# Kernel optimization log

Hardware: AMD Instinct MI355X
Metric: run time of the kernel (lower is better)

## Reference

```python
import jax, jax.numpy as jnp
import numpy as np


def _causal_kernel_mask(K):
    # casual_mask[i, K-i:] = 0 for i in 1..p
    p = K // 2
    m = np.ones((p + 1, K), np.float32)
    for i in range(1, p + 1):
        m[i, K - i:] = 0.0
    return jnp.asarray(m)


def setup_inputs() -> dict:
    rng = jax.random.key(0)
    k0, k1, k2, k3, k4 = jax.random.split(rng, 5)
    B, H, N, F = 2, 16, 1024, 64
    V, K = 32000, 5
    return {
        "input_ids": jax.random.randint(k0, (B, N), 0, V),
        "query": jax.random.normal(k1, (B, H, N, F), dtype=jnp.float32),
        "key": jax.random.normal(k2, (B, H, N, F), dtype=jnp.float32),
        "value": jax.random.normal(k3, (B, H, N, F), dtype=jnp.float32),
        "emb_weight": jax.random.normal(k4, (V, 2 * K), dtype=jnp.float32) * 0.02,
    }


def reference(input_ids, query, key, value, emb_weight):
    B, H, N, F = query.shape
    K = emb_weight.shape[1] // 2  # head/layer invariant -> emb dim = 2*K
    p = K // 2
    G = 2 * H

    # ---- get_kernel (layer 0; head_invariant + layer_invariant) ----
    kern = emb_weight[input_ids]                       # [B,N,2K]
    kern = kern.reshape(B, N, 2, 1, K)                 # [B,N,2,1,K]
    kern = jnp.broadcast_to(kern, (B, N, 2, H, K)).reshape(B, N, G, K)

    # ---- conv_key_value (for_casual=True, strict_on_casual=True) ----
    kv = jnp.concatenate([key, value], axis=1)         # [B,2H,N,F]
    kv_pad = jnp.pad(kv, ((0, 0), (0, 0), (p, p), (0, 0)))
    # unfold over token dim: [B,2H,K,N,F]
    kv_unf = jnp.stack([kv_pad[:, :, k:k + N, :] for k in range(K)], axis=2)
    cmask = _causal_kernel_mask(K)                     # [p+1,K]
    kern_m = kern[:, :, :, None, :] * cmask[None, None, None]  # [B,N,2H,p+1,K]
    # dynamic depthwise conv with per-offset causal masking
    out = jnp.einsum('bgknf,bngjk->bgjnf', kv_unf, kern_m)     # [B,2H,p+1,N,F]
    key_c = out[:, :H, 0]                              # [B,H,N,F]
    value_c = out[:, H:, 0]                            # [B,H,N,F]

    # ---- attention with causal-boundary corrections (n_past = 0) ----
    scale = 1.0 / jnp.sqrt(jnp.asarray(F, dtype=query.dtype))
    q = query * scale
    scores = jnp.einsum('bhnf,bhmf->bhnm', q, key_c)   # [B,H,N,N]

    # correct_attn_weights_near_casual_boundary
    for i in range(p):
        off = p - 1 - i
        cb_key = out[:, :H, 1 + i]                     # [B,H,N,F]
        corr = jnp.einsum('bhnf,bhnf->bhn', q[:, :, off:, :], cb_key[:, :, :N - off, :])
        rows = jnp.arange(N - off) + off
        cols = jnp.arange(N - off)
        scores = scores.at[:, :, rows, cols].set(corr)

    causal = jnp.tril(jnp.ones((N, N), dtype=bool))
    scores = jnp.where(causal, scores, jnp.asarray(-1e9, dtype=scores.dtype))
    probs = jax.nn.softmax(scores, axis=-1)
    attn = jnp.einsum('bhnm,bhmf->bhnf', probs, value_c)

    # correct_attn_output_near_casual_boundary
    for i in range(p):
        off = p - 1 - i
        cb_value = out[:, H:, 1 + i]                   # [B,H,N,F]
        idx = jnp.arange(N - off)
        diag_w = probs[:, :, idx + off, idx]           # diag offset=-off: [B,H,N-off]
        diff_v = cb_value[:, :, :N - off, :] - value_c[:, :, :N - off, :]
        diff = diag_w[..., None] * diff_v
        attn = attn + jnp.pad(diff, ((0, 0), (0, 0), (off, 0), (0, 0)))

    return attn
```

## Files before the change

kernel.cpp:

```cpp
#include <hip/hip_runtime.h>

#define HD    64
#define NSEQ  1024
#define NPB   12
#define CROWS 32
#define LOG2E 1.44269504088896f

typedef __attribute__((ext_vector_type(8))) __bf16 bf16x8;
typedef __attribute__((ext_vector_type(4))) float  f32x4;
typedef __attribute__((ext_vector_type(4))) unsigned short u16x4;

__device__ __constant__ unsigned char PAIRS12[NPB] = {
    6, 8, 10, 12, 14, 15, 4, 13, 2, 11, 0, 9 };

__device__ inline unsigned short f2bf(float x) {
    unsigned u = __float_as_uint(x);
    return (unsigned short)((u + 0x7fffu + ((u >> 16) & 1u)) >> 16);
}
__device__ inline unsigned pk2(float a, float b) {
    return (unsigned)f2bf(a) | ((unsigned)f2bf(b) << 16);
}
__device__ inline float dot4(f32x4 a, f32x4 b) {
    return a.x * b.x + a.y * b.y + a.z * b.z + a.w * b.w;
}

__global__ __launch_bounds__(256) void conv_kernel(
    const int* __restrict__ ids,
    const float* __restrict__ keyg,
    const float* __restrict__ valg,
    const float* __restrict__ qg,
    const float* __restrict__ emb,
    unsigned short* __restrict__ kc,
    unsigned short* __restrict__ vcT,
    float* __restrict__ dg1, float* __restrict__ dg2)
{
    __shared__ float se[(CROWS + 1) * 10];
    __shared__ float vtile[CROWS][68];
    int pid = blockIdx.x;
    int bh = pid & 31;
    int n0 = (pid >> 5) * CROWS;
    int b  = bh >> 4;
    int t  = threadIdx.x;
    size_t hb = (size_t)bh * NSEQ * HD;

    for (int u = t; u < (CROWS + 1) * 10; u += 256) {
        int r = u / 10, c = u - r * 10;
        int n = n0 - 1 + r;
        se[u] = (n >= 0) ? emb[(size_t)ids[b * NSEQ + n] * 10 + c] : 0.f;
    }
    __syncthreads();

    const float* kb = keyg + hb;
    const float* vb = valg + hb;
#pragma unroll
    for (int i = 0; i < 2; ++i) {
        int u  = (i << 8) + t;
        int nl = u >> 4, g4 = u & 15;
        int n  = n0 + nl, f = g4 << 2;
        const float* e  = se + (nl + 1) * 10;
        const float* ep = se + nl * 10;
        f32x4 xk[5], xv[5];
#pragma unroll
        for (int k = 0; k < 5; ++k) {
            int m = n + k - 2;
            if (m >= 0 && m < NSEQ) {
                xk[k] = *(const f32x4*)(kb + (size_t)m * HD + f);
                xv[k] = *(const f32x4*)(vb + (size_t)m * HD + f);
            } else {
                xk[k] = (f32x4){0.f, 0.f, 0.f, 0.f};
                xv[k] = (f32x4){0.f, 0.f, 0.f, 0.f};
            }
        }
        f32x4 km3 = (n >= 3) ? *(const f32x4*)(kb + (size_t)(n - 3) * HD + f)
                             : (f32x4){0.f, 0.f, 0.f, 0.f};
        f32x4 qv = *(const f32x4*)(qg + hb + (size_t)n * HD + f) * (0.125f * LOG2E);

        f32x4 k012 = e[0] * xk[0] + e[1] * xk[1] + e[2] * xk[2];
        f32x4 kcv  = k012 + e[3] * xk[3] + e[4] * xk[4];
        f32x4 vcv  = e[5] * xv[0] + e[6] * xv[1] + e[7] * xv[2] + e[8] * xv[3] + e[9] * xv[4];

        u16x4 kq;
        kq.x = f2bf(kcv.x); kq.y = f2bf(kcv.y); kq.z = f2bf(kcv.z); kq.w = f2bf(kcv.w);
        *(u16x4*)(kc + hb + (size_t)n * HD + f) = kq;
        *(f32x4*)(&vtile[nl][f]) = vcv;

        float s2 = dot4(qv, k012);
        f32x4 kj1 = ep[0] * km3 + ep[1] * xk[0] + ep[2] * xk[1] + ep[3] * xk[2];
        float s1 = dot4(qv, kj1);
#pragma unroll
        for (int o = 1; o < 16; o <<= 1) {
            s2 += __shfl_xor(s2, o, 64);
            s1 += __shfl_xor(s1, o, 64);
        }
        if (g4 == 0) {
            dg2[bh * NSEQ + n] = s2;
            dg1[bh * NSEQ + n] = s1;
        }
    }
    __syncthreads();
#pragma unroll
    for (int i = 0; i < 2; ++i) {
        int u = (i << 8) + t;
        int f = u >> 3, nn = (u & 7) << 2;
        u16x4 o;
        o.x = f2bf(vtile[nn + 0][f]);
        o.y = f2bf(vtile[nn + 1][f]);
        o.z = f2bf(vtile[nn + 2][f]);
        o.w = f2bf(vtile[nn + 3][f]);
        *(u16x4*)(vcT + ((size_t)bh * HD + f) * NSEQ + n0 + nn) = o;
    }
}

__global__ __launch_bounds__(512, 4) void attn_kernel(
    const float* __restrict__ qg,
    const unsigned short* __restrict__ kc,
    const unsigned short* __restrict__ vcT,
    const float* __restrict__ dg1, const float* __restrict__ dg2,
    const float* __restrict__ valg, const int* __restrict__ ids,
    const float* __restrict__ emb,
    float* __restrict__ pML, unsigned short* __restrict__ pO,
    float* __restrict__ outg)
{
    __shared__ __align__(16) unsigned char sK[8192];
    __shared__ __align__(16) unsigned char sV[8192];
    __shared__ __align__(16) unsigned char sP[16384];

    int pid  = blockIdx.x;
    int bh   = pid & 31;
    int slot = pid >> 5;
    int code = PAIRS12[slot];
    int jj = code >> 1, cch = code & 1;
    int t0 = cch << 3;
    int ntile = 2 * jj + 2;
    int len = cch ? (ntile - 8) : (ntile > 8 ? 8 : ntile);

    int t = threadIdx.x;
    int wv = t >> 6, l = t & 63;
    int w_in = wv & 3;
    int my_j = 2 * jj + (wv >> 2);
    int nc  = (my_j >= 8) ? 2 : 1;
    int lq = l & 15, h = l >> 4, l7 = l & 7;
    int lid = h * 16 + lq;
    int qbw = my_j * 64 + w_in * 16;
    size_t hb = (size_t)bh * NSEQ * HD;

    const unsigned short* kcb = kc  + hb;
    const unsigned short* vtb = vcT + (size_t)bh * HD * NSEQ;

    bf16x8 qb0, qb1;
    {
        const float* qr = qg + hb + (size_t)(qbw + lq) * HD + 8 * h;
        f32x4 a0 = *(const f32x4*)(qr);
        f32x4 a1 = *(const f32x4*)(qr + 4);
        f32x4 b0 = *(const f32x4*)(qr + 32);
        f32x4 b1 = *(const f32x4*)(qr + 36);
        const float S = 0.125f * LOG2E;
        union { unsigned u[4]; bf16x8 v; } u0, u1;
        u0.u[0] = pk2(a0.x * S, a0.y * S); u0.u[1] = pk2(a0.z * S, a0.w * S);
        u0.u[2] = pk2(a1.x * S, a1.y * S); u0.u[3] = pk2(a1.z * S, a1.w * S);
        u1.u[0] = pk2(b0.x * S, b0.y * S); u1.u[1] = pk2(b0.z * S, b0.w * S);
        u1.u[2] = pk2(b1.x * S, b1.y * S); u1.u[3] = pk2(b1.z * S, b1.w * S);
        qb0 = u0.v; qb1 = u1.v;
    }
    float diag2_l = dg2[bh * NSEQ + qbw + lq];
    float diag1_l = dg1[bh * NSEQ + qbw + lq];

    f32x4 of[4];
#pragma unroll
    for (int ft = 0; ft < 4; ++ft) of[ft] = (f32x4){0.f, 0.f, 0.f, 0.f};
    float m_run = -1e30f, denom = 0.f;

    const int ka_off0 = ((0 + h) ^ l7) << 4;
    const int ka_off1 = ((4 + h) ^ l7) << 4;
    const int pr_base = wv * 2048 + lq * 128;
    const int chk0 = ((qbw > 0 ? qbw - 1 : 0) >> 6);

    uint4 pf[2];
    auto issue = [&](int tg) {
        int kv0 = tg << 6;
#pragma unroll
        for (int i = 0; i < 2; ++i) {
            int chunk = t + (i << 9);
            int buf = chunk >> 9, loc = chunk & 511;
            int r = loc >> 3, c = loc & 7;
            int cs = c ^ (r & 7);
            pf[i] = (buf == 0)
                ? *(const uint4*)(kcb + (size_t)(kv0 + r) * HD + cs * 8)
                : *(const uint4*)(vtb + (size_t)r * NSEQ + kv0 + cs * 8);
        }
    };
    auto commit = [&]() {
#pragma unroll
        for (int i = 0; i < 2; ++i) {
            int chunk = t + (i << 9);
            int buf = chunk >> 9, loc = chunk & 511;
            int r = loc >> 3, c = loc & 7;
            *(uint4*)((buf ? sV : sK) + r * 128 + c * 16) = pf[i];
        }
    };

    issue(t0); commit();
    for (int ti = 0; ti < len; ++ti) {
        __syncthreads();
        if (ti + 1 < len) issue(t0 + ti + 1);
        int tg  = t0 + ti;
        int kv0 = tg << 6;
        bool act = (tg <= my_j);

        if (act) {
            f32x4 p[4];
#pragma unroll
            for (int st = 0; st < 4; ++st) {
                bf16x8 ka0 = *(const bf16x8*)(sK + st * 2048 + lq * 128 + ka_off0);
                bf16x8 ka1 = *(const bf16x8*)(sK + st * 2048 + lq * 128 + ka_off1);
                f32x4 d = (f32x4){0.f, 0.f, 0.f, 0.f};
                d = __builtin_amdgcn_mfma_f32_16x16x32_bf16(ka0, qb0, d, 0, 0, 0);
                d = __builtin_amdgcn_mfma_f32_16x16x32_bf16(ka1, qb1, d, 0, 0, 0);
                p[st] = d;
            }

            if (tg >= chk0) {
                int n_l = qbw + lq;
#pragma unroll
                for (int st = 0; st < 4; ++st)
#pragma unroll
                    for (int r = 0; r < 4; ++r) {
                        int kv = kv0 + st * 16 + 4 * h + r;
                        float dd = p[st][r];
                        if (kv > n_l)           dd = -1e30f;
                        else if (kv == n_l)     dd = diag2_l;
                        else if (kv == n_l - 1) dd = diag1_l;
                        p[st][r] = dd;
                    }
            }

            float tmax = -1e30f;
#pragma unroll
            for (int st = 0; st < 4; ++st)
#pragma unroll
                for (int r = 0; r < 4; ++r) tmax = fmaxf(tmax, p[st][r]);
            tmax = fmaxf(tmax, __shfl_xor(tmax, 16, 64));
            tmax = fmaxf(tmax, __shfl_xor(tmax, 32, 64));
            if (!__all(tmax <= m_run + 7.0f)) {
                float m_new = fmaxf(m_run, tmax);
                float alpha = __builtin_exp2f(m_run - m_new);
                denom *= alpha;
                m_run = m_new;
#pragma unroll
                for (int r = 0; r < 4; ++r) {
                    float ar = __shfl(alpha, 4 * h + r, 64);
                    of[0][r] *= ar; of[1][r] *= ar; of[2][r] *= ar; of[3][r] *= ar;
                }
            }
            float lsum = 0.f;
#pragma unroll
            for (int st = 0; st < 4; ++st)
#pragma unroll
                for (int r = 0; r < 4; ++r) {
                    float e = __builtin_exp2f(p[st][r] - m_run);
                    p[st][r] = e;
                    lsum += e;
                }
            lsum += __shfl_xor(lsum, 16, 64);
            lsum += __shfl_xor(lsum, 32, 64);
            denom += lsum;

#pragma unroll
            for (int st = 0; st < 4; ++st) {
                uint2 uu;
                uu.x = pk2(p[st][0], p[st][1]);
                uu.y = pk2(p[st][2], p[st][3]);
                int chunk = (st << 1) + (h >> 1);
                *(uint2*)(sP + pr_base + ((chunk ^ l7) << 4) + ((h & 1) << 3)) = uu;
            }
            asm volatile("s_waitcnt lgkmcnt(0)" ::: "memory");
            __builtin_amdgcn_sched_barrier(0);

#pragma unroll
            for (int kk = 0; kk < 2; ++kk) {
                int koff = kk ? ka_off1 : ka_off0;
                bf16x8 pa = *(const bf16x8*)(sP + pr_base + koff);
#pragma unroll
                for (int ft = 0; ft < 4; ++ft) {
                    bf16x8 vb = *(const bf16x8*)(sV + ft * 2048 + lq * 128 + koff);
                    of[ft] = __builtin_amdgcn_mfma_f32_16x16x32_bf16(pa, vb, of[ft], 0, 0, 0);
                }
            }
        }
        __syncthreads();
        if (ti + 1 < len) commit();
    }

    int psBase = ((bh << 4) | my_j) << 2;
    if (nc > 1) {
        if (h == 0) {
            float2 ml; ml.x = m_run; ml.y = denom;
            *(float2*)(pML + ((size_t)(psBase + cch) * 64 + w_in * 16 + lq) * 2) = ml;
        }
#pragma unroll
        for (int ft = 0; ft < 4; ++ft)
#pragma unroll
            for (int r = 0; r < 4; ++r)
                pO[(size_t)((((psBase + cch) * 4 + w_in) * 4 + ft) * 4 + r) * 64 + lid] =
                    f2bf(of[ft][r]);
        return;
    }

    const float* vraw = valg + hb;
    float* outr = outg + hb;
    const int* idb = ids + (size_t)(bh >> 4) * NSEQ;
#pragma unroll
    for (int r = 0; r < 4; ++r) {
        int qrow = 4 * h + r;
        int n = qbw + qrow;
        float dn = __shfl(denom,   qrow, 64);
        float mf = __shfl(m_run,   qrow, 64);
        float d2 = __shfl(diag2_l, qrow, 64);
        float d1 = __shfl(diag1_l, qrow, 64);
        float inv = 1.0f / dn;
        float p2 = __builtin_exp2f(d2 - mf) * inv;
        float p1 = (n >= 1) ? __builtin_exp2f(d1 - mf) * inv : 0.f;
        int id_n = idb[n];
        float e8  = emb[(size_t)id_n * 10 + 8];
        float e9  = emb[(size_t)id_n * 10 + 9];
        float e9p = (n >= 1) ? emb[(size_t)idb[n - 1] * 10 + 9] : 0.f;
        float ca = -(p2 * e8 + p1 * e9p);
        float cb = -p2 * e9;
#pragma unroll
        for (int ft = 0; ft < 4; ++ft) {
            int f = ft * 16 + lq;
            float v = of[ft][r] * inv;
            if (n + 1 < NSEQ) v += ca * vraw[(size_t)(n + 1) * HD + f];
            if (n + 2 < NSEQ) v += cb * vraw[(size_t)(n + 2) * HD + f];
            outr[(size_t)n * HD + f] = v;
        }
    }
}

__global__ __launch_bounds__(256) void merge_kernel(
    const float* __restrict__ pML, const unsigned short* __restrict__ pO,
    const float* __restrict__ dg1, const float* __restrict__ dg2,
    const float* __restrict__ valg, const int* __restrict__ ids,
    const float* __restrict__ emb, float* __restrict__ outg)
{
    int pid = blockIdx.x;
    int bh = pid & 31, j = (pid >> 5) + 8;
    int t = threadIdx.x;
    int rloc = t >> 2, fg = t & 3;
    int n = (j << 6) + rloc;
    int f0 = fg << 4;
    size_t hb = (size_t)bh * NSEQ * HD;
    int psBase = ((bh << 4) | j) << 2;

    float mc[2], lc[2];
#pragma unroll
    for (int c = 0; c < 2; ++c) {
        float2 v = *(const float2*)(pML + ((size_t)(psBase + c) * 64 + rloc) * 2);
        mc[c] = v.x; lc[c] = v.y;
    }
    float mg = fmaxf(mc[0], mc[1]);
    float D = 0.f;
    f32x4 a0 = (f32x4){0.f,0.f,0.f,0.f}, a1 = a0, a2 = a0, a3 = a0;
#pragma unroll
    for (int c = 0; c < 2; ++c) {
        float wc = __builtin_exp2f(mc[c] - mg);
        D += lc[c] * wc;
        const unsigned short* pp = pO +
            (size_t)((((psBase + c) * 4 + (rloc >> 4)) * 4 + fg) * 4 + (rloc & 3)) * 64
            + ((rloc >> 2) & 3) * 16;
        uint4 ua = *(const uint4*)(pp);
        uint4 ub = *(const uint4*)(pp + 8);
        a0.x += wc * __uint_as_float(ua.x << 16);
        a0.y += wc * __uint_as_float(ua.x & 0xffff0000u);
        a0.z += wc * __uint_as_float(ua.y << 16);
        a0.w += wc * __uint_as_float(ua.y & 0xffff0000u);
        a1.x += wc * __uint_as_float(ua.z << 16);
        a1.y += wc * __uint_as_float(ua.z & 0xffff0000u);
        a1.z += wc * __uint_as_float(ua.w << 16);
        a1.w += wc * __uint_as_float(ua.w & 0xffff0000u);
        a2.x += wc * __uint_as_float(ub.x << 16);
        a2.y += wc * __uint_as_float(ub.x & 0xffff0000u);
        a2.z += wc * __uint_as_float(ub.y << 16);
        a2.w += wc * __uint_as_float(ub.y & 0xffff0000u);
        a3.x += wc * __uint_as_float(ub.z << 16);
        a3.y += wc * __uint_as_float(ub.z & 0xffff0000u);
        a3.z += wc * __uint_as_float(ub.w << 16);
        a3.w += wc * __uint_as_float(ub.w & 0xffff0000u);
    }
    float inv = 1.0f / D;
    float d2 = dg2[bh * NSEQ + n], d1 = dg1[bh * NSEQ + n];
    float p2 = __builtin_exp2f(d2 - mg) * inv;
    float p1 = __builtin_exp2f(d1 - mg) * inv;
    const int* idb = ids + (size_t)(bh >> 4) * NSEQ;
    int id_n = idb[n];
    float e8  = emb[(size_t)id_n * 10 + 8];
    float e9  = emb[(size_t)id_n * 10 + 9];
    float e9p = emb[(size_t)idb[n - 1] * 10 + 9];
    float ca = -(p2 * e8 + p1 * e9p);
    float cb = -p2 * e9;

    a0 *= inv; a1 *= inv; a2 *= inv; a3 *= inv;
    if (n + 1 < NSEQ) {
        const float* v1 = valg + hb + (size_t)(n + 1) * HD + f0;
        a0 += ca * *(const f32x4*)(v1);
        a1 += ca * *(const f32x4*)(v1 + 4);
        a2 += ca * *(const f32x4*)(v1 + 8);
        a3 += ca * *(const f32x4*)(v1 + 12);
    }
    if (n + 2 < NSEQ) {
        const float* v2 = valg + hb + (size_t)(n + 2) * HD + f0;
        a0 += cb * *(const f32x4*)(v2);
        a1 += cb * *(const f32x4*)(v2 + 4);
        a2 += cb * *(const f32x4*)(v2 + 8);
        a3 += cb * *(const f32x4*)(v2 + 12);
    }
    float* o = outg + hb + (size_t)n * HD + f0;
    *(f32x4*)(o)      = a0;
    *(f32x4*)(o + 4)  = a1;
    *(f32x4*)(o + 8)  = a2;
    *(f32x4*)(o + 12) = a3;
}

extern "C" void kernel_launch(void* const* d_in, const int* in_sizes, int n_in,
                              void* d_out, int out_size, void* d_ws, size_t ws_size,
                              hipStream_t stream)
{
    const int*   ids = (const int*)  d_in[0];
    const float* q   = (const float*)d_in[1];
    const float* key = (const float*)d_in[2];
    const float* val = (const float*)d_in[3];
    const float* emb = (const float*)d_in[4];
    float* out = (float*)d_out;

    char* w = (char*)d_ws;
    unsigned short* kc  = (unsigned short*)(w);
    unsigned short* vcT = (unsigned short*)(w + (4u << 20));
    float* dg1 = (float*)(w + 8388608);
    float* dg2 = (float*)(w + 8519680);
    float* pML = (float*)(w + 8650752);
    unsigned short* pO = (unsigned short*)(w + 9699328);

    conv_kernel<<<1024, 256, 0, stream>>>(ids, key, val, q, emb, kc, vcT, dg1, dg2);
    attn_kernel<<<32 * NPB, 512, 0, stream>>>(q, kc, vcT, dg1, dg2, val, ids, emb,
                                              pML, pO, out);
    merge_kernel<<<256, 256, 0, stream>>>(pML, pO, dg1, dg2, val, ids, emb, out);
}
```

Measured before the change: 55.08 us.

## Double-buffer K/V tiles in LDS and raise wave priority around MFMA

New measurement: 54.84 us. Within noise of the previous version (-0.4%).

```diff
diff --git a/kernel.cpp b/kernel.cpp
--- a/kernel.cpp
+++ b/kernel.cpp
@@ -121,8 +121,8 @@
     float* __restrict__ pML, unsigned short* __restrict__ pO,
     float* __restrict__ outg)
 {
-    __shared__ __align__(16) unsigned char sK[8192];
-    __shared__ __align__(16) unsigned char sV[8192];
+    __shared__ __align__(16) unsigned char sK[2][8192];
+    __shared__ __align__(16) unsigned char sV[2][8192];
     __shared__ __align__(16) unsigned char sP[16384];
 
     int pid  = blockIdx.x;
@@ -175,49 +175,55 @@
     const int pr_base = wv * 2048 + lq * 128;
     const int chk0 = ((qbw > 0 ? qbw - 1 : 0) >> 6);
 
+    const int s_r0 = (t & 511) >> 3, s_c0 = t & 7;
+    const int s_cs0 = s_c0 ^ (s_r0 & 7);
+    const int s_buf0 = t >> 9;
+    const int s_r1 = ((t + 512) & 511) >> 3, s_c1 = (t + 512) & 7;
+    const int s_cs1 = s_c1 ^ (s_r1 & 7);
+    const int s_buf1 = (t + 512) >> 9;
+
     uint4 pf[2];
     auto issue = [&](int tg) {
         int kv0 = tg << 6;
-#pragma unroll
-        for (int i = 0; i < 2; ++i) {
-            int chunk = t + (i << 9);
-            int buf = chunk >> 9, loc = chunk & 511;
-            int r = loc >> 3, c = loc & 7;
-            int cs = c ^ (r & 7);
-            pf[i] = (buf == 0)
-                ? *(const uint4*)(kcb + (size_t)(kv0 + r) * HD + cs * 8)
-                : *(const uint4*)(vtb + (size_t)r * NSEQ + kv0 + cs * 8);
-        }
+        pf[0] = (s_buf0 == 0)
+            ? *(const uint4*)(kcb + (size_t)(kv0 + s_r0) * HD + s_cs0 * 8)
+            : *(const uint4*)(vtb + (size_t)s_r0 * NSEQ + kv0 + s_cs0 * 8);
+        pf[1] = (s_buf1 == 0)
+            ? *(const uint4*)(kcb + (size_t)(kv0 + s_r1) * HD + s_cs1 * 8)
+            : *(const uint4*)(vtb + (size_t)s_r1 * NSEQ + kv0 + s_cs1 * 8);
     };
-    auto commit = [&]() {
-#pragma unroll
-        for (int i = 0; i < 2; ++i) {
-            int chunk = t + (i << 9);
-            int buf = chunk >> 9, loc = chunk & 511;
-            int r = loc >> 3, c = loc & 7;
-            *(uint4*)((buf ? sV : sK) + r * 128 + c * 16) = pf[i];
-        }
+    auto commit = [&](int cu) {
+        *(uint4*)((s_buf0 ? sV[cu] : sK[cu]) + s_r0 * 128 + s_c0 * 16) = pf[0];
+        *(uint4*)((s_buf1 ? sV[cu] : sK[cu]) + s_r1 * 128 + s_c1 * 16) = pf[1];
     };
 
-    issue(t0); commit();
+    issue(t0); commit(0);
+    if (len > 1) issue(t0 + 1);
+    __syncthreads();
+
     for (int ti = 0; ti < len; ++ti) {
-        __syncthreads();
-        if (ti + 1 < len) issue(t0 + ti + 1);
+        int cur = ti & 1;
+        if (ti + 1 < len) commit(cur ^ 1);
+        if (ti + 2 < len) issue(t0 + ti + 2);
         int tg  = t0 + ti;
         int kv0 = tg << 6;
         bool act = (tg <= my_j);
 
         if (act) {
+            const unsigned char* sKc = sK[cur];
+            const unsigned char* sVc = sV[cur];
             f32x4 p[4];
+            __builtin_amdgcn_s_setprio(1);
 #pragma unroll
             for (int st = 0; st < 4; ++st) {
-                bf16x8 ka0 = *(const bf16x8*)(sK + st * 2048 + lq * 128 + ka_off0);
-                bf16x8 ka1 = *(const bf16x8*)(sK + st * 2048 + lq * 128 + ka_off1);
+                bf16x8 ka0 = *(const bf16x8*)(sKc + st * 2048 + lq * 128 + ka_off0);
+                bf16x8 ka1 = *(const bf16x8*)(sKc + st * 2048 + lq * 128 + ka_off1);
                 f32x4 d = (f32x4){0.f, 0.f, 0.f, 0.f};
                 d = __builtin_amdgcn_mfma_f32_16x16x32_bf16(ka0, qb0, d, 0, 0, 0);
                 d = __builtin_amdgcn_mfma_f32_16x16x32_bf16(ka1, qb1, d, 0, 0, 0);
                 p[st] = d;
             }
+            __builtin_amdgcn_s_setprio(0);
 
             if (tg >= chk0) {
                 int n_l = qbw + lq;
@@ -276,19 +282,20 @@
             asm volatile("s_waitcnt lgkmcnt(0)" ::: "memory");
             __builtin_amdgcn_sched_barrier(0);
 
+            __builtin_amdgcn_s_setprio(1);
 #pragma unroll
             for (int kk = 0; kk < 2; ++kk) {
                 int koff = kk ? ka_off1 : ka_off0;
                 bf16x8 pa = *(const bf16x8*)(sP + pr_base + koff);
 #pragma unroll
                 for (int ft = 0; ft < 4; ++ft) {
-                    bf16x8 vb = *(const bf16x8*)(sV + ft * 2048 + lq * 128 + koff);
+                    bf16x8 vb = *(const bf16x8*)(sVc + ft * 2048 + lq * 128 + koff);
                     of[ft] = __builtin_amdgcn_mfma_f32_16x16x32_bf16(pa, vb, of[ft], 0, 0, 0);
                 }
             }
-        }
-        __syncthreads();
-        if (ti + 1 < len) commit();
+            __builtin_amdgcn_s_setprio(0);
+        }
+        if (ti + 1 < len) __syncthreads();
     }
 
     int psBase = ((bh << 4) | my_j) << 2;
```
